# Performance work log

Hardware: AMD Instinct MI355X
Metric: run time of the kernel (lower is better)

The kernel has to match this reference:

```python
import jax, jax.numpy as jnp
import numpy as np

N_NODES = 50000
N_EDGES = 800000
D = 128


def setup_inputs() -> dict:
    key = jax.random.key(0)
    ks = jax.random.split(key, 8)
    x = jax.random.normal(ks[0], (N_NODES, D), dtype=jnp.float32)
    src = jax.random.randint(ks[1], (N_EDGES,), 0, N_NODES, dtype=jnp.int64)
    dst = jax.random.randint(ks[2], (N_EDGES,), 0, N_NODES, dtype=jnp.int64)
    edge_weights = jax.random.uniform(ks[3], (N_EDGES,), dtype=jnp.float32)
    scale = 1.0 / np.sqrt(D)
    W1 = jax.random.normal(ks[4], (D, D), dtype=jnp.float32) * scale
    b1 = jnp.zeros((D,), dtype=jnp.float32)
    W2 = jax.random.normal(ks[5], (D, D), dtype=jnp.float32) * scale
    b2 = jnp.zeros((D,), dtype=jnp.float32)
    return {"x": x, "src": src, "dst": dst, "edge_weights": edge_weights,
            "W1": W1, "b1": b1, "W2": W2, "b2": b2}


def reference(x, src, dst, edge_weights, W1, b1, W2, b2):
    n_nodes = x.shape[0]
    # out-degrees (edges where node is the source), clamped to >= 1
    deg = jax.ops.segment_sum(jnp.ones_like(src, dtype=x.dtype), src,
                              num_segments=n_nodes)
    deg = jnp.maximum(deg, 1.0)
    # per-edge symmetric-normalization coefficient: 1/sqrt(deg_u * deg_v)
    coef = jax.lax.rsqrt(deg[src] * deg[dst]) * edge_weights  # [E]
    # gather-multiply-scatter: sum_{u->v} x[u] * coef into node v
    msgs = x[src] * coef[:, None]                              # [E, D]
    agg = jax.ops.segment_sum(msgs, dst, num_segments=n_nodes)  # [N, D]
    # FFN: Linear -> ReLU -> Linear (dropout = 0)
    h = jax.nn.relu(agg @ W1 + b1)
    return h @ W2 + b2
```

## Files before the change

### kernel.cpp

```cpp
#include <hip/hip_runtime.h>

#define NN 50000
#define NE 800000
#define D  128
#define NBLK ((NN + 255) / 256)
#define HB 128
#define CH 6272
#define PW 50176

typedef short short8 __attribute__((ext_vector_type(8)));
typedef float f32x4  __attribute__((ext_vector_type(4)));
typedef unsigned char u8;

__device__ __forceinline__ ushort f2bf(float f) {
    union { float f; unsigned u; } v; v.f = f;
    unsigned r = v.u + 0x7FFFu + ((v.u >> 16) & 1u);
    return (ushort)(r >> 16);
}


__global__ __launch_bounds__(1024) void hist_kernel(const int* __restrict__ src,
                                                    const int* __restrict__ dst,
                                                    u8* __restrict__ psrc,
                                                    u8* __restrict__ pdst) {
    __shared__ unsigned bins[2 * PW / 4];
    const int t = threadIdx.x, b = blockIdx.x;
    for (int i = t; i < 2 * PW / 16; i += 1024)
        ((uint4*)bins)[i] = make_uint4(0, 0, 0, 0);
    __syncthreads();

    const int base = b * CH;
#pragma unroll
    for (int i = 0; i < 2; ++i) {
        int e0 = base + i * 4096 + t * 4;
        if (e0 < base + CH && e0 < NE) {
            int4 s4 = *(const int4*)(src + e0);
            int4 d4 = *(const int4*)(dst + e0);
            atomicAdd(&bins[s4.x >> 2], 1u << ((s4.x & 3) << 3));
            atomicAdd(&bins[s4.y >> 2], 1u << ((s4.y & 3) << 3));
            atomicAdd(&bins[s4.z >> 2], 1u << ((s4.z & 3) << 3));
            atomicAdd(&bins[s4.w >> 2], 1u << ((s4.w & 3) << 3));
            atomicAdd(&bins[PW / 4 + (d4.x >> 2)], 1u << ((d4.x & 3) << 3));
            atomicAdd(&bins[PW / 4 + (d4.y >> 2)], 1u << ((d4.y & 3) << 3));
            atomicAdd(&bins[PW / 4 + (d4.z >> 2)], 1u << ((d4.z & 3) << 3));
            atomicAdd(&bins[PW / 4 + (d4.w >> 2)], 1u << ((d4.w & 3) << 3));
        }
    }
    __syncthreads();
    uint4* os = (uint4*)(psrc + (size_t)b * PW);
    uint4* od = (uint4*)(pdst + (size_t)b * PW);
    for (int i = t; i < PW / 16; i += 1024) {
        os[i] = ((const uint4*)bins)[i];
        od[i] = ((const uint4*)(bins + PW / 4))[i];
    }
}


__global__ __launch_bounds__(256) void reduce_kernel(const unsigned* __restrict__ psrc32,
                                                     unsigned* __restrict__ pdst32,
                                                     float* __restrict__ rsq,
                                                     int* __restrict__ cnt) {
    int g = blockIdx.x * 256 + threadIdx.x;
    if (g >= PW / 4) return;
    unsigned s02 = 0, s13 = 0;
    for (int b = 0; b < HB; ++b) {
        unsigned w = psrc32[(size_t)b * (PW / 4) + g];
        s02 += w & 0x00FF00FFu;
        s13 += (w >> 8) & 0x00FF00FFu;
    }
    unsigned r02 = 0, r13 = 0;
    for (int b = 0; b < HB; ++b) {
        size_t idx = (size_t)b * (PW / 4) + g;
        unsigned w = pdst32[idx];
        pdst32[idx] = (r02 & 0xFFu) | ((r13 & 0xFFu) << 8) |
                      (r02 & 0x00FF0000u) | ((r13 & 0x00FF0000u) << 8);
        r02 += w & 0x00FF00FFu;
        r13 += (w >> 8) & 0x00FF00FFu;
    }
    int v0 = g * 4;
    int dg[4] = { (int)(s02 & 0xFFFFu), (int)(s13 & 0xFFFFu),
                  (int)(s02 >> 16),     (int)(s13 >> 16) };
    int ct[4] = { (int)(r02 & 0xFFFFu), (int)(r13 & 0xFFFFu),
                  (int)(r02 >> 16),     (int)(r13 >> 16) };
    if (v0 + 3 < NN) {
        float4 rq = make_float4(rsqrtf(fmaxf((float)dg[0], 1.f)),
                                rsqrtf(fmaxf((float)dg[1], 1.f)),
                                rsqrtf(fmaxf((float)dg[2], 1.f)),
                                rsqrtf(fmaxf((float)dg[3], 1.f)));
        *(float4*)(rsq + v0) = rq;
        *(int4*)(cnt + v0) = make_int4(ct[0], ct[1], ct[2], ct[3]);
    } else {
        for (int j = 0; j < 4; ++j)
            if (v0 + j < NN) {
                rsq[v0 + j] = rsqrtf(fmaxf((float)dg[j], 1.f));
                cnt[v0 + j] = ct[j];
            }
    }
}


__global__ __launch_bounds__(256) void scan_partial(const int* __restrict__ cnt,
                                                    int* __restrict__ bsum) {
    __shared__ int sm[256];
    int t = threadIdx.x;
    int i = blockIdx.x * 256 + t;
    sm[t] = (i < NN) ? cnt[i] : 0;
    __syncthreads();
    for (int s = 128; s > 0; s >>= 1) {
        if (t < s) sm[t] += sm[t + s];
        __syncthreads();
    }
    if (t == 0) bsum[blockIdx.x] = sm[0];
}

__global__ __launch_bounds__(256) void scan_bsum(int* __restrict__ bsum) {
    __shared__ int sm[256];
    int t = threadIdx.x;
    int v = (t < NBLK) ? bsum[t] : 0;
    sm[t] = v;
    __syncthreads();
    for (int d2 = 1; d2 < 256; d2 <<= 1) {
        int u = (t >= d2) ? sm[t - d2] : 0;
        __syncthreads();
        sm[t] += u;
        __syncthreads();
    }
    if (t < NBLK) bsum[t] = sm[t] - v;
}

__global__ __launch_bounds__(256) void scan_write(const int* __restrict__ cnt,
                                                  const int* __restrict__ bsum,
                                                  int* __restrict__ offs) {
    __shared__ int sm[256];
    int b = blockIdx.x, t = threadIdx.x;
    int i = b * 256 + t;
    int v = (i < NN) ? cnt[i] : 0;
    sm[t] = v;
    __syncthreads();
    for (int d2 = 1; d2 < 256; d2 <<= 1) {
        int u = (t >= d2) ? sm[t - d2] : 0;
        __syncthreads();
        sm[t] += u;
        __syncthreads();
    }
    if (i < NN) offs[i] = bsum[b] + sm[t] - v;
    if (b == 0 && t == 0) offs[NN] = NE;
}


__global__ __launch_bounds__(1024) void scatter_kernel(const int* __restrict__ src,
                                                       const int* __restrict__ dst,
                                                       const float* __restrict__ ew,
                                                       const float* __restrict__ rsq,
                                                       const int* __restrict__ offs,
                                                       const u8* __restrict__ pd,
                                                       unsigned* __restrict__ csr) {
    __shared__ unsigned cur[PW / 4];
    const int t = threadIdx.x, b = blockIdx.x;
    for (int i = t; i < PW / 16; i += 1024)
        ((uint4*)cur)[i] = make_uint4(0, 0, 0, 0);
    __syncthreads();

    const u8* pdrow = pd + (size_t)b * PW;
    const int base = b * CH;
#pragma unroll
    for (int i = 0; i < 2; ++i) {
        int e0 = base + i * 4096 + t * 4;
        if (e0 < base + CH && e0 < NE) {
            int4 s4 = *(const int4*)(src + e0);
            int4 d4 = *(const int4*)(dst + e0);
            float4 w4 = *(const float4*)(ew + e0);
#pragma unroll
            for (int j = 0; j < 4; ++j) {
                int s = (j == 0) ? s4.x : (j == 1) ? s4.y : (j == 2) ? s4.z : s4.w;
                int d = (j == 0) ? d4.x : (j == 1) ? d4.y : (j == 2) ? d4.z : d4.w;
                float w = (j == 0) ? w4.x : (j == 1) ? w4.y : (j == 2) ? w4.z : w4.w;
                int sh = (d & 3) << 3;
                unsigned old = atomicAdd(&cur[d >> 2], 1u << sh);
                int rel = (int)((old >> sh) & 0xFFu);
                int pos = offs[d] + (int)pdrow[d] + rel;
                float coef = rsq[s] * rsq[d] * w;
                csr[pos] = (unsigned)s | ((unsigned)f2bf(coef) << 16);
            }
        }
    }
}


__global__ __launch_bounds__(256) void xprep_kernel(const float* __restrict__ x,
                                                    ushort* __restrict__ xbf) {
    int i = blockIdx.x * 256 + threadIdx.x;
    if (i >= NN * D / 8) return;
    const float4* p = (const float4*)(x + (size_t)i * 8);
    float4 v0 = p[0], v1 = p[1];
    ushort tmp[8];
    tmp[0] = f2bf(v0.x); tmp[1] = f2bf(v0.y); tmp[2] = f2bf(v0.z); tmp[3] = f2bf(v0.w);
    tmp[4] = f2bf(v1.x); tmp[5] = f2bf(v1.y); tmp[6] = f2bf(v1.z); tmp[7] = f2bf(v1.w);
    *reinterpret_cast<uint4*>(xbf + (size_t)i * 8) = *reinterpret_cast<uint4*>(tmp);
}


__global__ __launch_bounds__(256) void gather_bf16_kernel(const int* __restrict__ offs,
                                                          const unsigned* __restrict__ csr,
                                                          const ushort* __restrict__ xbf,
                                                          float* __restrict__ agg) {
    int v = blockIdx.x * 8 + (threadIdx.x >> 5);
    if (v >= NN) return;
    int lane = threadIdx.x & 31;
    int beg = offs[v], end = offs[v + 1];
    float a0 = 0.f, a1 = 0.f, a2 = 0.f, a3 = 0.f;
    for (int i0 = beg; i0 < end; i0 += 32) {
        int n = end - i0; if (n > 32) n = 32;
        unsigned ej = (lane < n) ? csr[i0 + lane] : 0u;
        for (int j = 0; j < n; ++j) {
            unsigned e = __shfl(ej, j, 32);
            int s = (int)(e & 0xFFFFu);
            float c = __int_as_float(e & 0xFFFF0000u);
            uint2 u = ((const uint2*)(xbf + (size_t)s * D))[lane];
            float x0 = __int_as_float((int)(u.x << 16));
            float x1 = __int_as_float((int)(u.x & 0xFFFF0000u));
            float x2 = __int_as_float((int)(u.y << 16));
            float x3 = __int_as_float((int)(u.y & 0xFFFF0000u));
            a0 = fmaf(x0, c, a0);
            a1 = fmaf(x1, c, a1);
            a2 = fmaf(x2, c, a2);
            a3 = fmaf(x3, c, a3);
        }
    }
    ((float4*)(agg + (size_t)v * D))[lane] = make_float4(a0, a1, a2, a3);
}


__global__ __launch_bounds__(256) void wprep_kernel(const float* __restrict__ W1,
                                                    const float* __restrict__ W2,
                                                    ushort* __restrict__ W1t,
                                                    ushort* __restrict__ W2t) {
    int c = blockIdx.x * 256 + threadIdx.x;
    const float* W = (c < 2048) ? W1 : W2;
    ushort* Wt     = (c < 2048) ? W1t : W2t;
    int cc = c & 2047;
    int n  = cc >> 4;
    int k0 = (cc & 15) * 8;
    ushort tmp[8];
#pragma unroll
    for (int j = 0; j < 8; ++j) tmp[j] = f2bf(W[(k0 + j) * D + n]);
    *reinterpret_cast<uint4*>(Wt + n * D + k0) = *reinterpret_cast<uint4*>(tmp);
}


__global__ __launch_bounds__(256) void ffn_mfma_kernel(const float* __restrict__ agg,
                                                       const ushort* __restrict__ W1t,
                                                       const ushort* __restrict__ W2t,
                                                       const float* __restrict__ b1,
                                                       const float* __restrict__ b2,
                                                       float* __restrict__ out) {
    __shared__ ushort Wt[128 * 128];
    __shared__ ushort hS[4][16 * 128];

    const int t  = threadIdx.x;
    const int w  = t >> 6;
    const int l  = t & 63;
    const int lr = l & 15;
    const int lk = l >> 4;
    const int r0 = blockIdx.x * 64;

    for (int i = 0; i < 8; ++i) {
        int c = i * 256 + t;
        int n = c >> 4;
        int slot = c & 15;
        uint4 v = ((const uint4*)W1t)[c];
        int byte = n * 256 + ((slot * 16) ^ ((n & 7) << 4));
        *(uint4*)((char*)Wt + byte) = v;
    }

    const int arow = r0 + w * 16 + lr;
    short8 afrag[4];
#pragma unroll
    for (int kb = 0; kb < 4; ++kb) {
        int k = kb * 32 + lk * 8;
        float4 v0 = make_float4(0.f, 0.f, 0.f, 0.f), v1 = v0;
        if (arow < NN) {
            const float4* ap = (const float4*)(agg + (size_t)arow * D + k);
            v0 = ap[0]; v1 = ap[1];
        }
        short8 a;
        a[0] = (short)f2bf(v0.x); a[1] = (short)f2bf(v0.y);
        a[2] = (short)f2bf(v0.z); a[3] = (short)f2bf(v0.w);
        a[4] = (short)f2bf(v1.x); a[5] = (short)f2bf(v1.y);
        a[6] = (short)f2bf(v1.z); a[7] = (short)f2bf(v1.w);
        afrag[kb] = a;
    }
    __syncthreads();

    f32x4 acc[8];
#pragma unroll
    for (int nt = 0; nt < 8; ++nt) acc[nt] = (f32x4){0.f, 0.f, 0.f, 0.f};
#pragma unroll
    for (int kb = 0; kb < 4; ++kb) {
        int kbyte = (kb * 32 + lk * 8) * 2;
#pragma unroll
        for (int nt = 0; nt < 8; ++nt) {
            int n = nt * 16 + lr;
            short8 b = *(const short8*)((const char*)Wt + n * 256 + (kbyte ^ ((n & 7) << 4)));
            acc[nt] = __builtin_amdgcn_mfma_f32_16x16x32_bf16(afrag[kb], b, acc[nt], 0, 0, 0);
        }
    }
#pragma unroll
    for (int nt = 0; nt < 8; ++nt) {
        int col = nt * 16 + lr;
        float bb = b1[col];
#pragma unroll
        for (int r = 0; r < 4; ++r) {
            int row = lk * 4 + r;
            float h = fmaxf(acc[nt][r] + bb, 0.0f);
            int byte = row * 256 + ((col * 2) ^ ((row & 7) << 4));
            *(ushort*)((char*)&hS[w][0] + byte) = f2bf(h);
        }
    }
    __syncthreads();

    for (int i = 0; i < 8; ++i) {
        int c = i * 256 + t;
        int n = c >> 4;
        int slot = c & 15;
        uint4 v = ((const uint4*)W2t)[c];
        int byte = n * 256 + ((slot * 16) ^ ((n & 7) << 4));
        *(uint4*)((char*)Wt + byte) = v;
    }
    __syncthreads();

    short8 hfrag[4];
#pragma unroll
    for (int kb = 0; kb < 4; ++kb) {
        int kbyte = (kb * 32 + lk * 8) * 2;
        hfrag[kb] = *(const short8*)((const char*)&hS[w][0] + lr * 256 + (kbyte ^ ((lr & 7) << 4)));
    }
#pragma unroll
    for (int nt = 0; nt < 8; ++nt) acc[nt] = (f32x4){0.f, 0.f, 0.f, 0.f};
#pragma unroll
    for (int kb = 0; kb < 4; ++kb) {
        int kbyte = (kb * 32 + lk * 8) * 2;
#pragma unroll
        for (int nt = 0; nt < 8; ++nt) {
            int n = nt * 16 + lr;
            short8 b = *(const short8*)((const char*)Wt + n * 256 + (kbyte ^ ((n & 7) << 4)));
            acc[nt] = __builtin_amdgcn_mfma_f32_16x16x32_bf16(hfrag[kb], b, acc[nt], 0, 0, 0);
        }
    }
#pragma unroll
    for (int nt = 0; nt < 8; ++nt) {
        int col = nt * 16 + lr;
        float bb = b2[col];
#pragma unroll
        for (int r = 0; r < 4; ++r) {
            int row = r0 + w * 16 + lk * 4 + r;
            if (row < NN) out[(size_t)row * D + col] = acc[nt][r] + bb;
        }
    }
}


extern "C" void kernel_launch(void* const* d_in, const int* in_sizes, int n_in,
                              void* d_out, int out_size, void* d_ws, size_t ws_size,
                              hipStream_t stream) {
    const float* x  = (const float*)d_in[0];
    const int* src  = (const int*)d_in[1];
    const int* dst  = (const int*)d_in[2];
    const float* ew = (const float*)d_in[3];
    const float* W1 = (const float*)d_in[4];
    const float* b1 = (const float*)d_in[5];
    const float* W2 = (const float*)d_in[6];
    const float* b2 = (const float*)d_in[7];
    float* out = (float*)d_out;

    char* base = (char*)d_ws;
    size_t off = 0;
    auto alloc = [&](size_t bytes) { char* p = base + off; off = (off + bytes + 15) & ~(size_t)15; return p; };
    u8* psrc      = (u8*)alloc((size_t)HB * PW);
    u8* pdst      = (u8*)alloc((size_t)HB * PW);
    float* rsq    = (float*)alloc((size_t)NN * 4);
    int* cnt      = (int*)alloc((size_t)NN * 4);
    int* offs     = (int*)alloc((size_t)(NN + 1) * 4);
    int* bsum     = (int*)alloc((size_t)NBLK * 4);
    unsigned* csr = (unsigned*)alloc((size_t)NE * 4);
    ushort* W1t   = (ushort*)alloc((size_t)D * D * 2);
    ushort* W2t   = (ushort*)alloc((size_t)D * D * 2);
    ushort* xbf   = (ushort*)psrc;

    wprep_kernel<<<16, 256, 0, stream>>>(W1, W2, W1t, W2t);
    hist_kernel<<<HB, 1024, 0, stream>>>(src, dst, psrc, pdst);
    reduce_kernel<<<(PW / 4 + 255) / 256, 256, 0, stream>>>((const unsigned*)psrc,
                                                            (unsigned*)pdst, rsq, cnt);
    scan_partial<<<NBLK, 256, 0, stream>>>(cnt, bsum);
    scan_bsum<<<1, 256, 0, stream>>>(bsum);
    scan_write<<<NBLK, 256, 0, stream>>>(cnt, bsum, offs);
    scatter_kernel<<<HB, 1024, 0, stream>>>(src, dst, ew, rsq, offs, pdst, csr);
    xprep_kernel<<<(NN * D / 8 + 255) / 256, 256, 0, stream>>>(x, xbf);
    gather_bf16_kernel<<<(NN + 7) / 8, 256, 0, stream>>>(offs, csr, xbf, out);
    ffn_mfma_kernel<<<(NN + 63) / 64, 256, 0, stream>>>(out, W1t, W2t, b1, b2, out);
}
```

Baseline: 138.4 us.

## Fuse histogram, weight prep and x conversion into one prep kernel

Result: no change. 137.1 us (-1.0%).

```diff
diff --git a/kernel.cpp b/kernel.cpp
--- a/kernel.cpp
+++ b/kernel.cpp
@@ -3,10 +3,11 @@
 #define NN 50000
 #define NE 800000
 #define D  128
-#define NBLK ((NN + 255) / 256)
 #define HB 128
 #define CH 6272
 #define PW 50176
+#define XB 128
+#define RB 49
 
 typedef short short8 __attribute__((ext_vector_type(8)));
 typedef float f32x4  __attribute__((ext_vector_type(4)));
@@ -19,49 +20,93 @@
 }
 
 
-__global__ __launch_bounds__(1024) void hist_kernel(const int* __restrict__ src,
+__global__ __launch_bounds__(1024) void prep_kernel(const int* __restrict__ src,
                                                     const int* __restrict__ dst,
+                                                    const float* __restrict__ x,
+                                                    const float* __restrict__ W1,
+                                                    const float* __restrict__ W2,
                                                     u8* __restrict__ psrc,
-                                                    u8* __restrict__ pdst) {
+                                                    u8* __restrict__ pdst,
+                                                    ushort* __restrict__ xbf,
+                                                    ushort* __restrict__ W1t,
+                                                    ushort* __restrict__ W2t) {
     __shared__ unsigned bins[2 * PW / 4];
     const int t = threadIdx.x, b = blockIdx.x;
-    for (int i = t; i < 2 * PW / 16; i += 1024)
-        ((uint4*)bins)[i] = make_uint4(0, 0, 0, 0);
-    __syncthreads();
-
-    const int base = b * CH;
-#pragma unroll
-    for (int i = 0; i < 2; ++i) {
-        int e0 = base + i * 4096 + t * 4;
-        if (e0 < base + CH && e0 < NE) {
-            int4 s4 = *(const int4*)(src + e0);
-            int4 d4 = *(const int4*)(dst + e0);
-            atomicAdd(&bins[s4.x >> 2], 1u << ((s4.x & 3) << 3));
-            atomicAdd(&bins[s4.y >> 2], 1u << ((s4.y & 3) << 3));
-            atomicAdd(&bins[s4.z >> 2], 1u << ((s4.z & 3) << 3));
-            atomicAdd(&bins[s4.w >> 2], 1u << ((s4.w & 3) << 3));
-            atomicAdd(&bins[PW / 4 + (d4.x >> 2)], 1u << ((d4.x & 3) << 3));
-            atomicAdd(&bins[PW / 4 + (d4.y >> 2)], 1u << ((d4.y & 3) << 3));
-            atomicAdd(&bins[PW / 4 + (d4.z >> 2)], 1u << ((d4.z & 3) << 3));
-            atomicAdd(&bins[PW / 4 + (d4.w >> 2)], 1u << ((d4.w & 3) << 3));
-        }
-    }
-    __syncthreads();
-    uint4* os = (uint4*)(psrc + (size_t)b * PW);
-    uint4* od = (uint4*)(pdst + (size_t)b * PW);
-    for (int i = t; i < PW / 16; i += 1024) {
-        os[i] = ((const uint4*)bins)[i];
-        od[i] = ((const uint4*)(bins + PW / 4))[i];
-    }
+
+    if (b < HB) {
+        for (int i = t; i < 2 * PW / 16; i += 1024)
+            ((uint4*)bins)[i] = make_uint4(0, 0, 0, 0);
+        __syncthreads();
+        const int base = b * CH;
+#pragma unroll
+        for (int i = 0; i < 2; ++i) {
+            int e0 = base + i * 4096 + t * 4;
+            if (e0 < base + CH && e0 < NE) {
+                int4 s4 = *(const int4*)(src + e0);
+                int4 d4 = *(const int4*)(dst + e0);
+                atomicAdd(&bins[s4.x >> 2], 1u << ((s4.x & 3) << 3));
+                atomicAdd(&bins[s4.y >> 2], 1u << ((s4.y & 3) << 3));
+                atomicAdd(&bins[s4.z >> 2], 1u << ((s4.z & 3) << 3));
+                atomicAdd(&bins[s4.w >> 2], 1u << ((s4.w & 3) << 3));
+                atomicAdd(&bins[PW / 4 + (d4.x >> 2)], 1u << ((d4.x & 3) << 3));
+                atomicAdd(&bins[PW / 4 + (d4.y >> 2)], 1u << ((d4.y & 3) << 3));
+                atomicAdd(&bins[PW / 4 + (d4.z >> 2)], 1u << ((d4.z & 3) << 3));
+                atomicAdd(&bins[PW / 4 + (d4.w >> 2)], 1u << ((d4.w & 3) << 3));
+            }
+        }
+        __syncthreads();
+        uint4* os = (uint4*)(psrc + (size_t)b * PW);
+        uint4* od = (uint4*)(pdst + (size_t)b * PW);
+        for (int i = t; i < PW / 16; i += 1024) {
+            os[i] = ((const uint4*)bins)[i];
+            od[i] = ((const uint4*)(bins + PW / 4))[i];
+        }
+    } else if (b < HB + 4) {
+        int c = (b - HB) * 1024 + t;
+        if (c < 4096) {
+            const float* W = (c < 2048) ? W1 : W2;
+            ushort* Wt     = (c < 2048) ? W1t : W2t;
+            int cc = c & 2047;
+            int n  = cc >> 4;
+            int k0 = (cc & 15) * 8;
+            ushort tmp[8];
+#pragma unroll
+            for (int j = 0; j < 8; ++j) tmp[j] = f2bf(W[(k0 + j) * D + n]);
+            *reinterpret_cast<uint4*>(Wt + n * D + k0) = *reinterpret_cast<uint4*>(tmp);
+        }
+    } else {
+        for (int i = (b - HB - 4) * 1024 + t; i < NN * D / 8; i += XB * 1024) {
+            const float4* p = (const float4*)(x + (size_t)i * 8);
+            float4 v0 = p[0], v1 = p[1];
+            ushort tmp[8];
+            tmp[0] = f2bf(v0.x); tmp[1] = f2bf(v0.y); tmp[2] = f2bf(v0.z); tmp[3] = f2bf(v0.w);
+            tmp[4] = f2bf(v1.x); tmp[5] = f2bf(v1.y); tmp[6] = f2bf(v1.z); tmp[7] = f2bf(v1.w);
+            *reinterpret_cast<uint4*>(xbf + (size_t)i * 8) = *reinterpret_cast<uint4*>(tmp);
+        }
+    }
+}
+
+__global__ __launch_bounds__(256) void xprep_kernel(const float* __restrict__ x,
+                                                    ushort* __restrict__ xbf) {
+    int i = blockIdx.x * 256 + threadIdx.x;
+    if (i >= NN * D / 8) return;
+    const float4* p = (const float4*)(x + (size_t)i * 8);
+    float4 v0 = p[0], v1 = p[1];
+    ushort tmp[8];
+    tmp[0] = f2bf(v0.x); tmp[1] = f2bf(v0.y); tmp[2] = f2bf(v0.z); tmp[3] = f2bf(v0.w);
+    tmp[4] = f2bf(v1.x); tmp[5] = f2bf(v1.y); tmp[6] = f2bf(v1.z); tmp[7] = f2bf(v1.w);
+    *reinterpret_cast<uint4*>(xbf + (size_t)i * 8) = *reinterpret_cast<uint4*>(tmp);
 }
 
 
 __global__ __launch_bounds__(256) void reduce_kernel(const unsigned* __restrict__ psrc32,
                                                      unsigned* __restrict__ pdst32,
                                                      float* __restrict__ rsq,
-                                                     int* __restrict__ cnt) {
-    int g = blockIdx.x * 256 + threadIdx.x;
-    if (g >= PW / 4) return;
+                                                     int* __restrict__ cnt,
+                                                     int* __restrict__ bsum49) {
+    __shared__ int sm[256];
+    int t = threadIdx.x;
+    int g = blockIdx.x * 256 + t;
     unsigned s02 = 0, s13 = 0;
     for (int b = 0; b < HB; ++b) {
         unsigned w = psrc32[(size_t)b * (PW / 4) + g];
@@ -96,27 +141,23 @@
                 cnt[v0 + j] = ct[j];
             }
     }
-}
-
-
-__global__ __launch_bounds__(256) void scan_partial(const int* __restrict__ cnt,
-                                                    int* __restrict__ bsum) {
+    int pad_ok = (v0 + 3 < NN);
+    int mysum = pad_ok ? (ct[0] + ct[1] + ct[2] + ct[3]) : 0;
+    if (!pad_ok)
+        for (int j = 0; j < 4; ++j) if (v0 + j < NN) mysum += ct[j];
+    sm[t] = mysum;
+    __syncthreads();
+    for (int s = 128; s > 0; s >>= 1) {
+        if (t < s) sm[t] += sm[t + s];
+        __syncthreads();
+    }
+    if (t == 0) bsum49[blockIdx.x] = sm[0];
+}
+
+__global__ __launch_bounds__(256) void scan_bsum(int* __restrict__ bsum49) {
     __shared__ int sm[256];
     int t = threadIdx.x;
-    int i = blockIdx.x * 256 + t;
-    sm[t] = (i < NN) ? cnt[i] : 0;
-    __syncthreads();
-    for (int s = 128; s > 0; s >>= 1) {
-        if (t < s) sm[t] += sm[t + s];
-        __syncthreads();
-    }
-    if (t == 0) bsum[blockIdx.x] = sm[0];
-}
-
-__global__ __launch_bounds__(256) void scan_bsum(int* __restrict__ bsum) {
-    __shared__ int sm[256];
-    int t = threadIdx.x;
-    int v = (t < NBLK) ? bsum[t] : 0;
+    int v = (t < RB) ? bsum49[t] : 0;
     sm[t] = v;
     __syncthreads();
     for (int d2 = 1; d2 < 256; d2 <<= 1) {
@@ -125,25 +166,25 @@
         sm[t] += u;
         __syncthreads();
     }
-    if (t < NBLK) bsum[t] = sm[t] - v;
-}
-
-__global__ __launch_bounds__(256) void scan_write(const int* __restrict__ cnt,
-                                                  const int* __restrict__ bsum,
-                                                  int* __restrict__ offs) {
-    __shared__ int sm[256];
+    if (t < RB) bsum49[t] = sm[t] - v;
+}
+
+__global__ __launch_bounds__(1024) void scan_write(const int* __restrict__ cnt,
+                                                   const int* __restrict__ bsum49,
+                                                   int* __restrict__ offs) {
+    __shared__ int sm[1024];
     int b = blockIdx.x, t = threadIdx.x;
-    int i = b * 256 + t;
+    int i = b * 1024 + t;
     int v = (i < NN) ? cnt[i] : 0;
     sm[t] = v;
     __syncthreads();
-    for (int d2 = 1; d2 < 256; d2 <<= 1) {
+    for (int d2 = 1; d2 < 1024; d2 <<= 1) {
         int u = (t >= d2) ? sm[t - d2] : 0;
         __syncthreads();
         sm[t] += u;
         __syncthreads();
     }
-    if (i < NN) offs[i] = bsum[b] + sm[t] - v;
+    if (i < NN) offs[i] = bsum49[b] + sm[t] - v;
     if (b == 0 && t == 0) offs[NN] = NE;
 }
 
@@ -187,18 +228,16 @@
 }
 
 
-__global__ __launch_bounds__(256) void xprep_kernel(const float* __restrict__ x,
-                                                    ushort* __restrict__ xbf) {
-    int i = blockIdx.x * 256 + threadIdx.x;
-    if (i >= NN * D / 8) return;
-    const float4* p = (const float4*)(x + (size_t)i * 8);
-    float4 v0 = p[0], v1 = p[1];
-    ushort tmp[8];
-    tmp[0] = f2bf(v0.x); tmp[1] = f2bf(v0.y); tmp[2] = f2bf(v0.z); tmp[3] = f2bf(v0.w);
-    tmp[4] = f2bf(v1.x); tmp[5] = f2bf(v1.y); tmp[6] = f2bf(v1.z); tmp[7] = f2bf(v1.w);
-    *reinterpret_cast<uint4*>(xbf + (size_t)i * 8) = *reinterpret_cast<uint4*>(tmp);
-}
-
+__device__ __forceinline__ void acc_row(unsigned e, int lane,
+                                        const ushort* __restrict__ xbf,
+                                        float& a0, float& a1, float& a2, float& a3) {
+    float c = __int_as_float(e & 0xFFFF0000u);
+    uint2 u = ((const uint2*)(xbf + (size_t)(e & 0xFFFFu) * D))[lane];
+    a0 = fmaf(__int_as_float((int)(u.x << 16)),        c, a0);
+    a1 = fmaf(__int_as_float((int)(u.x & 0xFFFF0000u)), c, a1);
+    a2 = fmaf(__int_as_float((int)(u.y << 16)),        c, a2);
+    a3 = fmaf(__int_as_float((int)(u.y & 0xFFFF0000u)), c, a3);
+}
 
 __global__ __launch_bounds__(256) void gather_bf16_kernel(const int* __restrict__ offs,
                                                           const unsigned* __restrict__ csr,
@@ -212,39 +251,44 @@
     for (int i0 = beg; i0 < end; i0 += 32) {
         int n = end - i0; if (n > 32) n = 32;
         unsigned ej = (lane < n) ? csr[i0 + lane] : 0u;
-        for (int j = 0; j < n; ++j) {
+        int j = 0;
+        for (; j + 3 < n; j += 4) {
+            unsigned e0 = __shfl(ej, j,     32);
+            unsigned e1 = __shfl(ej, j + 1, 32);
+            unsigned e2 = __shfl(ej, j + 2, 32);
+            unsigned e3 = __shfl(ej, j + 3, 32);
+            const uint2* r0 = (const uint2*)(xbf + (size_t)(e0 & 0xFFFFu) * D);
+            const uint2* r1 = (const uint2*)(xbf + (size_t)(e1 & 0xFFFFu) * D);
+            const uint2* r2 = (const uint2*)(xbf + (size_t)(e2 & 0xFFFFu) * D);
+            const uint2* r3 = (const uint2*)(xbf + (size_t)(e3 & 0xFFFFu) * D);
+            uint2 u0 = r0[lane], u1 = r1[lane], u2 = r2[lane], u3 = r3[lane];
+            float c0 = __int_as_float(e0 & 0xFFFF0000u);
+            float c1 = __int_as_float(e1 & 0xFFFF0000u);
+            float c2 = __int_as_float(e2 & 0xFFFF0000u);
+            float c3 = __int_as_float(e3 & 0xFFFF0000u);
+            a0 = fmaf(__int_as_float((int)(u0.x << 16)),         c0, a0);
+            a1 = fmaf(__int_as_float((int)(u0.x & 0xFFFF0000u)), c0, a1);
+            a2 = fmaf(__int_as_float((int)(u0.y << 16)),         c0, a2);
+            a3 = fmaf(__int_as_float((int)(u0.y & 0xFFFF0000u)), c0, a3);
+            a0 = fmaf(__int_as_float((int)(u1.x << 16)),         c1, a0);
+            a1 = fmaf(__int_as_float((int)(u1.x & 0xFFFF0000u)), c1, a1);
+            a2 = fmaf(__int_as_float((int)(u1.y << 16)),         c1, a2);
+            a3 = fmaf(__int_as_float((int)(u1.y & 0xFFFF0000u)), c1, a3);
+            a0 = fmaf(__int_as_float((int)(u2.x << 16)),         c2, a0);
+            a1 = fmaf(__int_as_float((int)(u2.x & 0xFFFF0000u)), c2, a1);
+            a2 = fmaf(__int_as_float((int)(u2.y << 16)),         c2, a2);
+            a3 = fmaf(__int_as_float((int)(u2.y & 0xFFFF0000u)), c2, a3);
+            a0 = fmaf(__int_as_float((int)(u3.x << 16)),         c3, a0);
+            a1 = fmaf(__int_as_float((int)(u3.x & 0xFFFF0000u)), c3, a1);
+            a2 = fmaf(__int_as_float((int)(u3.y << 16)),         c3, a2);
+            a3 = fmaf(__int_as_float((int)(u3.y & 0xFFFF0000u)), c3, a3);
+        }
+        for (; j < n; ++j) {
             unsigned e = __shfl(ej, j, 32);
-            int s = (int)(e & 0xFFFFu);
-            float c = __int_as_float(e & 0xFFFF0000u);
-            uint2 u = ((const uint2*)(xbf + (size_t)s * D))[lane];
-            float x0 = __int_as_float((int)(u.x << 16));
-            float x1 = __int_as_float((int)(u.x & 0xFFFF0000u));
-            float x2 = __int_as_float((int)(u.y << 16));
-            float x3 = __int_as_float((int)(u.y & 0xFFFF0000u));
-            a0 = fmaf(x0, c, a0);
-            a1 = fmaf(x1, c, a1);
-            a2 = fmaf(x2, c, a2);
-            a3 = fmaf(x3, c, a3);
+            acc_row(e, lane, xbf, a0, a1, a2, a3);
         }
     }
     ((float4*)(agg + (size_t)v * D))[lane] = make_float4(a0, a1, a2, a3);
-}
-
-
-__global__ __launch_bounds__(256) void wprep_kernel(const float* __restrict__ W1,
-                                                    const float* __restrict__ W2,
-                                                    ushort* __restrict__ W1t,
-                                                    ushort* __restrict__ W2t) {
-    int c = blockIdx.x * 256 + threadIdx.x;
-    const float* W = (c < 2048) ? W1 : W2;
-    ushort* Wt     = (c < 2048) ? W1t : W2t;
-    int cc = c & 2047;
-    int n  = cc >> 4;
-    int k0 = (cc & 15) * 8;
-    ushort tmp[8];
-#pragma unroll
-    for (int j = 0; j < 8; ++j) tmp[j] = f2bf(W[(k0 + j) * D + n]);
-    *reinterpret_cast<uint4*>(Wt + n * D + k0) = *reinterpret_cast<uint4*>(tmp);
 }
 
 
@@ -381,21 +425,26 @@
     float* rsq    = (float*)alloc((size_t)NN * 4);
     int* cnt      = (int*)alloc((size_t)NN * 4);
     int* offs     = (int*)alloc((size_t)(NN + 1) * 4);
-    int* bsum     = (int*)alloc((size_t)NBLK * 4);
+    int* bsum49   = (int*)alloc((size_t)RB * 4);
     unsigned* csr = (unsigned*)alloc((size_t)NE * 4);
     ushort* W1t   = (ushort*)alloc((size_t)D * D * 2);
     ushort* W2t   = (ushort*)alloc((size_t)D * D * 2);
-    ushort* xbf   = (ushort*)psrc;
-
-    wprep_kernel<<<16, 256, 0, stream>>>(W1, W2, W1t, W2t);
-    hist_kernel<<<HB, 1024, 0, stream>>>(src, dst, psrc, pdst);
-    reduce_kernel<<<(PW / 4 + 255) / 256, 256, 0, stream>>>((const unsigned*)psrc,
-                                                            (unsigned*)pdst, rsq, cnt);
-    scan_partial<<<NBLK, 256, 0, stream>>>(cnt, bsum);
-    scan_bsum<<<1, 256, 0, stream>>>(bsum);
-    scan_write<<<NBLK, 256, 0, stream>>>(cnt, bsum, offs);
+    size_t off_noX = off;
+    ushort* xbf_own = (ushort*)alloc((size_t)NN * D * 2);
+    bool own_xbf = ws_size >= off;
+    ushort* xbf = own_xbf ? xbf_own : (ushort*)psrc;
+    (void)off_noX;
+
+    int prep_grid = own_xbf ? (HB + 4 + XB) : (HB + 4);
+    prep_kernel<<<prep_grid, 1024, 0, stream>>>(src, dst, x, W1, W2,
+                                                psrc, pdst, xbf, W1t, W2t);
+    reduce_kernel<<<RB, 256, 0, stream>>>((const unsigned*)psrc, (unsigned*)pdst,
+                                          rsq, cnt, bsum49);
+    scan_bsum<<<1, 256, 0, stream>>>(bsum49);
+    scan_write<<<RB, 1024, 0, stream>>>(cnt, bsum49, offs);
     scatter_kernel<<<HB, 1024, 0, stream>>>(src, dst, ew, rsq, offs, pdst, csr);
-    xprep_kernel<<<(NN * D / 8 + 255) / 256, 256, 0, stream>>>(x, xbf);
+    if (!own_xbf)
+        xprep_kernel<<<(NN * D / 8 + 255) / 256, 256, 0, stream>>>(x, xbf);
     gather_bf16_kernel<<<(NN + 7) / 8, 256, 0, stream>>>(offs, csr, xbf, out);
     ffn_mfma_kernel<<<(NN + 63) / 64, 256, 0, stream>>>(out, W1t, W2t, b1, b2, out);
 }
```
